# Kernel tuning notes

Hardware: AMD Instinct MI355X
Metric: run time of the kernel (lower is better)

## Reference

```python
import jax, jax.numpy as jnp
import numpy as np

B, D, H, W = 16, 512, 64, 64
K = 64  # clusters
EPS = 1e-12  # torch F.normalize eps


def _l2norm(v, axis):
    n = jnp.linalg.norm(v, axis=axis, keepdims=True)
    return v / jnp.maximum(n, EPS)


def setup_inputs() -> dict:
    key = jax.random.key(0)
    k1, k2, k3, k4 = jax.random.split(key, 4)
    x = jax.random.normal(k1, (B, D, H, W), dtype=jnp.float32)
    # conv weight/bias are independent trainable params after init; sample them
    centers = jax.random.uniform(k2, (K, D), dtype=jnp.float32)
    conv_w = 2.0 * 100.0 * centers + 0.01 * jax.random.normal(k3, (K, D), dtype=jnp.float32)
    conv_b = -100.0 * jnp.linalg.norm(centers, axis=1) + 0.01 * jax.random.normal(k4, (K,), dtype=jnp.float32)
    return {"x": x, "conv_w": conv_w, "conv_b": conv_b, "centers": centers}


def reference(x, conv_w, conv_b, centers):
    b = x.shape[0]
    x_flat = x.reshape(b, D, -1)                       # (B, D, N)
    # 1x1 conv == per-location linear over channels
    logits = jnp.einsum('bdn,kd->bkn', x_flat, conv_w) + conv_b[None, :, None]
    w = jax.nn.softmax(logits, axis=1)                 # softmax over clusters
    # vlad[b,k,d] = sum_n w[b,k,n]*(x[b,d,n] - c[k,d])
    #            = (w @ x^T)[b,k,d] - (sum_n w[b,k,n]) * c[k,d]
    wx = jnp.einsum('bkn,bdn->bkd', w, x_flat)         # (B, K, D)
    wsum = jnp.sum(w, axis=-1)                          # (B, K)
    vlad = wx - wsum[:, :, None] * centers[None]        # (B, K, D)
    vlad = _l2norm(vlad, axis=2)                        # intra-normalize
    vlad = vlad.reshape(b, -1)
    vlad = _l2norm(vlad, axis=1)                        # global L2
    return vlad
```

## Files before the change

### kernel.cpp

```cpp
#include <hip/hip_runtime.h>
#include <hip/hip_bf16.h>
#include <math.h>

#define B_ 16
#define D_ 512
#define N_ 4096
#define K_ 64

typedef __attribute__((ext_vector_type(8))) short bfrag;
typedef __attribute__((ext_vector_type(4))) float f32x4;

static __device__ __forceinline__ float bf2f(unsigned short u) {
    return __uint_as_float(((unsigned)u) << 16);
}
static __device__ __forceinline__ unsigned short f2bf(float v) {
    __hip_bfloat16 h = __float2bfloat16(v);
    union { __hip_bfloat16 h; unsigned short u; } cv; cv.h = h; return cv.u;
}
static __device__ __forceinline__ void split3(float v, unsigned short& h,
                                              unsigned short& m, unsigned short& l) {
    h = f2bf(v); float r1 = v - bf2f(h);
    m = f2bf(r1); float r2 = r1 - bf2f(m);
    l = f2bf(r2);
}
static __device__ __forceinline__ void split2(float v, unsigned short& h,
                                              unsigned short& l) {
    h = f2bf(v); l = f2bf(v - bf2f(h));
}
#define MFMA(a, b, c) __builtin_amdgcn_mfma_f32_16x16x32_bf16((a), (b), (c), 0, 0, 0)

__global__ __launch_bounds__(256) void k_prep(
    const float* __restrict__ conv_w, unsigned short* __restrict__ cwL)
{
    const int i = blockIdx.x * 256 + threadIdx.x;
    const float4 v = *(const float4*)&conv_w[i * 4];
    const float vv[4] = {v.x, v.y, v.z, v.w};
    unsigned short h[4], m[4], l[4];
    #pragma unroll
    for (int j = 0; j < 4; ++j) split3(vv[j], h[j], m[j], l[j]);
    *(ushort4*)&cwL[0 * (K_ * D_) + i * 4] = make_ushort4(h[0], h[1], h[2], h[3]);
    *(ushort4*)&cwL[1 * (K_ * D_) + i * 4] = make_ushort4(m[0], m[1], m[2], m[3]);
    *(ushort4*)&cwL[2 * (K_ * D_) + i * 4] = make_ushort4(l[0], l[1], l[2], l[3]);
}

__global__ __launch_bounds__(256) void k_logits_softmax(
    const float* __restrict__ x, const unsigned short* __restrict__ cwL,
    const float* __restrict__ conv_b,
    unsigned short* __restrict__ wh, unsigned short* __restrict__ wl,
    float* __restrict__ wsumbuf)
{
    const int b   = blockIdx.x >> 5;
    const int n0  = (blockIdx.x & 31) * 128;
    const int tid  = threadIdx.x;
    const int w    = tid >> 6;
    const int lane = tid & 63;
    const int q = lane >> 4;
    const int c = lane & 15;
    const int ktb = (w & 1) * 32;
    const int ntb = (w >> 1) * 64;

    __shared__ unsigned short cws[3][64][40];
    __shared__ unsigned short xs[3][128][40];
    __shared__ float redm[2][128];
    __shared__ float reds[2][128];

    f32x4 acc[2][4];
    #pragma unroll
    for (int kt = 0; kt < 2; ++kt)
        #pragma unroll
        for (int nt = 0; nt < 4; ++nt) acc[kt][nt] = (f32x4){0.f, 0.f, 0.f, 0.f};

    const float* xb = x + (size_t)b * D_ * N_ + n0;

    const int ks = tid >> 2;
    const int d8 = (tid & 3) * 8;

    for (int d0 = 0; d0 < D_; d0 += 32) {
        #pragma unroll
        for (int lv = 0; lv < 3; ++lv)
            *(uint4*)&cws[lv][ks][d8] =
                *(const uint4*)&cwL[lv * (K_ * D_) + ks * D_ + d0 + d8];
        #pragma unroll
        for (int i = 0; i < 4; ++i) {
            const int s  = i * 256 + tid;
            const int xn = s & 127;
            const int j  = s >> 7;
            const int Cs = ((j >> 1) ^ ((xn >> 3) & 3));
            const int dsw = (Cs * 2 + (j & 1)) * 4;
            const int dg4 = j * 4;
            unsigned short h[4], m[4], l[4];
            #pragma unroll
            for (int r = 0; r < 4; ++r) {
                const float v = xb[(size_t)(d0 + dg4 + r) * N_ + xn];
                split3(v, h[r], m[r], l[r]);
            }
            *(ushort4*)&xs[0][xn][dsw] = make_ushort4(h[0], h[1], h[2], h[3]);
            *(ushort4*)&xs[1][xn][dsw] = make_ushort4(m[0], m[1], m[2], m[3]);
            *(ushort4*)&xs[2][xn][dsw] = make_ushort4(l[0], l[1], l[2], l[3]);
        }
        __syncthreads();

        bfrag af[2][3];
        #pragma unroll
        for (int kt = 0; kt < 2; ++kt)
            #pragma unroll
            for (int lv = 0; lv < 3; ++lv)
                af[kt][lv] = *(const bfrag*)&cws[lv][ktb + kt * 16 + c][q * 8];
        #pragma unroll
        for (int nt = 0; nt < 4; ++nt) {
            const int row = ntb + nt * 16 + c;
            const int qs  = (q ^ ((row >> 3) & 3)) * 8;
            bfrag bf[3];
            #pragma unroll
            for (int lv = 0; lv < 3; ++lv)
                bf[lv] = *(const bfrag*)&xs[lv][row][qs];
            #pragma unroll
            for (int kt = 0; kt < 2; ++kt) {
                f32x4 a = acc[kt][nt];
                a = MFMA(af[kt][0], bf[0], a);
                a = MFMA(af[kt][0], bf[1], a);
                a = MFMA(af[kt][1], bf[0], a);
                a = MFMA(af[kt][1], bf[1], a);
                a = MFMA(af[kt][0], bf[2], a);
                a = MFMA(af[kt][2], bf[0], a);
                acc[kt][nt] = a;
            }
        }
        __syncthreads();
    }

    #pragma unroll
    for (int kt = 0; kt < 2; ++kt)
        #pragma unroll
        for (int r = 0; r < 4; ++r) {
            const float bias = conv_b[ktb + kt * 16 + q * 4 + r];
            #pragma unroll
            for (int nt = 0; nt < 4; ++nt) acc[kt][nt][r] += bias;
        }

    float mloc[4];
    #pragma unroll
    for (int nt = 0; nt < 4; ++nt) {
        float m = acc[0][nt][0];
        #pragma unroll
        for (int kt = 0; kt < 2; ++kt)
            #pragma unroll
            for (int r = 0; r < 4; ++r) m = fmaxf(m, acc[kt][nt][r]);
        m = fmaxf(m, __shfl_xor(m, 16));
        m = fmaxf(m, __shfl_xor(m, 32));
        mloc[nt] = m;
    }
    if (q == 0)
        #pragma unroll
        for (int nt = 0; nt < 4; ++nt) redm[w & 1][ntb + nt * 16 + c] = mloc[nt];
    __syncthreads();
    float mall[4];
    #pragma unroll
    for (int nt = 0; nt < 4; ++nt)
        mall[nt] = fmaxf(redm[0][ntb + nt * 16 + c], redm[1][ntb + nt * 16 + c]);

    float sloc[4] = {0.f, 0.f, 0.f, 0.f};
    #pragma unroll
    for (int nt = 0; nt < 4; ++nt) {
        #pragma unroll
        for (int kt = 0; kt < 2; ++kt)
            #pragma unroll
            for (int r = 0; r < 4; ++r) {
                const float e = __expf(acc[kt][nt][r] - mall[nt]);
                acc[kt][nt][r] = e;
                sloc[nt] += e;
            }
        sloc[nt] += __shfl_xor(sloc[nt], 16);
        sloc[nt] += __shfl_xor(sloc[nt], 32);
    }
    if (q == 0)
        #pragma unroll
        for (int nt = 0; nt < 4; ++nt) reds[w & 1][ntb + nt * 16 + c] = sloc[nt];
    __syncthreads();

    float wacc[2][4] = {{0.f, 0.f, 0.f, 0.f}, {0.f, 0.f, 0.f, 0.f}};
    #pragma unroll
    for (int nt = 0; nt < 4; ++nt) {
        const float inv = 1.0f / (reds[0][ntb + nt * 16 + c] + reds[1][ntb + nt * 16 + c]);
        #pragma unroll
        for (int kt = 0; kt < 2; ++kt)
            #pragma unroll
            for (int r = 0; r < 4; ++r) {
                const float v = acc[kt][nt][r] * inv;
                unsigned short hi, lo;
                split2(v, hi, lo);
                const size_t idx = ((size_t)b * K_ + ktb + kt * 16 + q * 4 + r) * N_
                                 + n0 + ntb + nt * 16 + c;
                wh[idx] = hi;
                wl[idx] = lo;
                wacc[kt][r] += v;
            }
    }
    #pragma unroll
    for (int msk = 1; msk < 16; msk <<= 1)
        #pragma unroll
        for (int kt = 0; kt < 2; ++kt)
            #pragma unroll
            for (int r = 0; r < 4; ++r)
                wacc[kt][r] += __shfl_xor(wacc[kt][r], msk);
    if (c == 0)
        #pragma unroll
        for (int kt = 0; kt < 2; ++kt)
            #pragma unroll
            for (int r = 0; r < 4; ++r)
                atomicAdd(&wsumbuf[b * K_ + ktb + kt * 16 + q * 4 + r], wacc[kt][r]);
}

__global__ __launch_bounds__(256) void k_wx(
    const float* __restrict__ x, const unsigned short* __restrict__ wh,
    const unsigned short* __restrict__ wl, float* __restrict__ vlad)
{
    const int nc = blockIdx.x & 7;
    const int dc = (blockIdx.x >> 3) & 3;
    const int b  = blockIdx.x >> 5;
    const int tid  = threadIdx.x;
    const int w    = tid >> 6;
    const int lane = tid & 63;
    const int q = lane >> 4;
    const int c = lane & 15;
    const int ktb = (w & 1) * 32;
    const int dtb = (w >> 1) * 64;

    __shared__ unsigned short ws2[2][64][40];
    __shared__ unsigned short xs2[2][128][40];

    f32x4 acc[2][4];
    #pragma unroll
    for (int kt = 0; kt < 2; ++kt)
        #pragma unroll
        for (int dt = 0; dt < 4; ++dt) acc[kt][dt] = (f32x4){0.f, 0.f, 0.f, 0.f};

    const float* xb = x + (size_t)b * D_ * N_ + (size_t)dc * 128 * N_;
    const unsigned short* whb = wh + (size_t)b * K_ * N_;
    const unsigned short* wlb = wl + (size_t)b * K_ * N_;

    const int wk = tid >> 2;
    const int wn = (tid & 3) * 8;
    const int xd = tid >> 3;
    const int xn = (tid & 7) * 4;

    const int nbase = nc * 512;
    for (int n0 = nbase; n0 < nbase + 512; n0 += 32) {
        *(uint4*)&ws2[0][wk][wn] = *(const uint4*)&whb[(size_t)wk * N_ + n0 + wn];
        *(uint4*)&ws2[1][wk][wn] = *(const uint4*)&wlb[(size_t)wk * N_ + n0 + wn];
        #pragma unroll
        for (int i = 0; i < 4; ++i) {
            const float4 v = *(const float4*)&xb[(size_t)(i * 32 + xd) * N_ + n0 + xn];
            const float vv[4] = {v.x, v.y, v.z, v.w};
            unsigned short h[4], l[4];
            #pragma unroll
            for (int j = 0; j < 4; ++j) split2(vv[j], h[j], l[j]);
            *(ushort4*)&xs2[0][i * 32 + xd][xn] = make_ushort4(h[0], h[1], h[2], h[3]);
            *(ushort4*)&xs2[1][i * 32 + xd][xn] = make_ushort4(l[0], l[1], l[2], l[3]);
        }
        __syncthreads();

        bfrag afh[2], afl[2];
        #pragma unroll
        for (int kt = 0; kt < 2; ++kt) {
            afh[kt] = *(const bfrag*)&ws2[0][ktb + kt * 16 + c][q * 8];
            afl[kt] = *(const bfrag*)&ws2[1][ktb + kt * 16 + c][q * 8];
        }
        #pragma unroll
        for (int dt = 0; dt < 4; ++dt) {
            const bfrag bh = *(const bfrag*)&xs2[0][dtb + dt * 16 + c][q * 8];
            const bfrag bl = *(const bfrag*)&xs2[1][dtb + dt * 16 + c][q * 8];
            #pragma unroll
            for (int kt = 0; kt < 2; ++kt) {
                f32x4 a = acc[kt][dt];
                a = MFMA(afh[kt], bh, a);
                a = MFMA(afh[kt], bl, a);
                a = MFMA(afl[kt], bh, a);
                acc[kt][dt] = a;
            }
        }
        __syncthreads();
    }

    #pragma unroll
    for (int kt = 0; kt < 2; ++kt)
        #pragma unroll
        for (int dt = 0; dt < 4; ++dt)
            #pragma unroll
            for (int r = 0; r < 4; ++r) {
                const int k = ktb + kt * 16 + q * 4 + r;
                const int d = dc * 128 + dtb + dt * 16 + c;
                atomicAdd(&vlad[((size_t)b * K_ + k) * D_ + d], acc[kt][dt][r]);
            }
}

__global__ __launch_bounds__(256) void k_norm(
    const float* __restrict__ wsumbuf, const float* __restrict__ vlad,
    const float* __restrict__ centers, float* __restrict__ out)
{
    const int b = blockIdx.x >> 6;
    const int k = blockIdx.x & 63;
    const int tid = threadIdx.x;

    const float wsum = wsumbuf[b * K_ + k];

    const float* vr = vlad + ((size_t)b * K_ + k) * D_;
    const float* cr = centers + k * D_;
    const float v0 = vr[tid]       - wsum * cr[tid];
    const float v1 = vr[tid + 256] - wsum * cr[tid + 256];

    float ss = v0 * v0 + v1 * v1;
    __shared__ float red2[4];
    #pragma unroll
    for (int off = 32; off > 0; off >>= 1) ss += __shfl_down(ss, off, 64);
    if ((tid & 63) == 0) red2[tid >> 6] = ss;
    __syncthreads();
    const float nrm = sqrtf(red2[0] + red2[1] + red2[2] + red2[3]);
    const float scale = 1.0f / (8.0f * fmaxf(nrm, 1e-12f));

    float* outr = out + ((size_t)b * K_ + k) * D_;
    outr[tid]       = v0 * scale;
    outr[tid + 256] = v1 * scale;
}

extern "C" void kernel_launch(void* const* d_in, const int* in_sizes, int n_in,
                              void* d_out, int out_size, void* d_ws, size_t ws_size,
                              hipStream_t stream) {
    const float* x       = (const float*)d_in[0];
    const float* conv_w  = (const float*)d_in[1];
    const float* conv_b  = (const float*)d_in[2];
    const float* centers = (const float*)d_in[3];
    float* out = (float*)d_out;

    char* wsb = (char*)d_ws;
    float* vlad            = (float*)wsb;
    float* wsumbuf         = (float*)(wsb + (2u << 20));
    unsigned short* wh     = (unsigned short*)(wsb + (3u << 20));
    unsigned short* wl     = (unsigned short*)(wsb + (11u << 20));
    unsigned short* cwL    = (unsigned short*)(wsb + (19u << 20));

    hipMemsetAsync(vlad, 0, (2u << 20) + 4096, stream);

    k_prep<<<32, 256, 0, stream>>>(conv_w, cwL);
    k_logits_softmax<<<B_ * 32, 256, 0, stream>>>(x, cwL, conv_b, wh, wl, wsumbuf);
    k_wx<<<B_ * 4 * 8, 256, 0, stream>>>(x, wh, wl, vlad);
    k_norm<<<B_ * K_, 256, 0, stream>>>(wsumbuf, vlad, centers, out);
}
```

Baseline: 237.3 us.

## Fuse logits/softmax and weighted aggregation into one kernel using LDS-resident x tiles

Merges the logits+softmax kernel and the w·xᵀ kernel into a single kernel. Each block keeps a 512×64 fp32 x tile in LDS while computing logits, then reuses that tile for the aggregation MFMAs. This removes the second global read of x and the global round-trip of the bf16 hi/lo soft-assignment weights. Per-block partial VLAD sums are written to a workspace and reduced in the normalization kernel, replacing the atomics and the large memset. The cost is about 156KB of dynamic LDS per block, which allows only one 512-thread block per CU, and two barriers per 32-channel step, so the kernel may become latency bound.

```diff
diff --git a/kernel.cpp b/kernel.cpp
--- a/kernel.cpp
+++ b/kernel.cpp
@@ -28,6 +28,17 @@
     h = f2bf(v); l = f2bf(v - bf2f(h));
 }
 #define MFMA(a, b, c) __builtin_amdgcn_mfma_f32_16x16x32_bf16((a), (b), (c), 0, 0, 0)
+
+static __device__ __forceinline__ int xf_idx(int row, int col) {
+    const int CH  = col >> 2;
+    const int CHs = ((CH - 2 * (row & 7)) & 7) | (CH & 8);
+    return row * 68 + CHs * 4 + (col & 3);
+}
+static __device__ __forceinline__ int ws_idx(int k, int n) {
+    const int CH  = n >> 3;
+    const int CHs = (CH - 2 * (k & 7)) & 7;
+    return k * 72 + CHs * 8 + (n & 7);
+}
 
 __global__ __launch_bounds__(256) void k_prep(
     const float* __restrict__ conv_w, unsigned short* __restrict__ cwL)
@@ -43,271 +54,227 @@
     *(ushort4*)&cwL[2 * (K_ * D_) + i * 4] = make_ushort4(l[0], l[1], l[2], l[3]);
 }
 
-__global__ __launch_bounds__(256) void k_logits_softmax(
+__global__ __launch_bounds__(512, 2) void k_fused(
     const float* __restrict__ x, const unsigned short* __restrict__ cwL,
-    const float* __restrict__ conv_b,
-    unsigned short* __restrict__ wh, unsigned short* __restrict__ wl,
+    const float* __restrict__ conv_b, float* __restrict__ vlad_part,
     float* __restrict__ wsumbuf)
 {
-    const int b   = blockIdx.x >> 5;
-    const int n0  = (blockIdx.x & 31) * 128;
+    const int b    = blockIdx.x >> 4;
+    const int g    = blockIdx.x & 15;
     const int tid  = threadIdx.x;
     const int w    = tid >> 6;
     const int lane = tid & 63;
-    const int q = lane >> 4;
-    const int c = lane & 15;
-    const int ktb = (w & 1) * 32;
-    const int ntb = (w >> 1) * 64;
-
-    __shared__ unsigned short cws[3][64][40];
-    __shared__ unsigned short xs[3][128][40];
-    __shared__ float redm[2][128];
-    __shared__ float reds[2][128];
-
-    f32x4 acc[2][4];
-    #pragma unroll
-    for (int kt = 0; kt < 2; ++kt)
-        #pragma unroll
-        for (int nt = 0; nt < 4; ++nt) acc[kt][nt] = (f32x4){0.f, 0.f, 0.f, 0.f};
-
-    const float* xb = x + (size_t)b * D_ * N_ + n0;
-
-    const int ks = tid >> 2;
-    const int d8 = (tid & 3) * 8;
-
-    for (int d0 = 0; d0 < D_; d0 += 32) {
-        #pragma unroll
-        for (int lv = 0; lv < 3; ++lv)
-            *(uint4*)&cws[lv][ks][d8] =
-                *(const uint4*)&cwL[lv * (K_ * D_) + ks * D_ + d0 + d8];
-        #pragma unroll
-        for (int i = 0; i < 4; ++i) {
-            const int s  = i * 256 + tid;
-            const int xn = s & 127;
-            const int j  = s >> 7;
-            const int Cs = ((j >> 1) ^ ((xn >> 3) & 3));
-            const int dsw = (Cs * 2 + (j & 1)) * 4;
-            const int dg4 = j * 4;
+    const int q    = lane >> 4;
+    const int c    = lane & 15;
+    const int kw   = w >> 1;
+    const int nw   = w & 1;
+    const int dsub = w * 4;
+
+    extern __shared__ char smem[];
+    float*          xf   = (float*)smem;
+    unsigned short* xsb  = (unsigned short*)(smem + 139264);
+    unsigned short* wsb_ = (unsigned short*)(smem + 139264);
+    float*          redm = (float*)(smem + 157696);
+    float*          reds = (float*)(smem + 158720);
+
+    f32x4 acc2[16];
+    #pragma unroll
+    for (int i = 0; i < 16; ++i) acc2[i] = (f32x4){0.f, 0.f, 0.f, 0.f};
+    float wacc[4] = {0.f, 0.f, 0.f, 0.f};
+    float bias[4];
+    #pragma unroll
+    for (int r = 0; r < 4; ++r) bias[r] = conv_b[kw * 16 + q * 4 + r];
+
+    const unsigned short* cwp = cwL + (kw * 16 + c) * D_ + q * 8;
+
+    #pragma unroll 1
+    for (int t = 0; t < 4; ++t) {
+        const int gn0 = g * 256 + t * 64;
+        const float* xb = x + (size_t)b * ((size_t)D_ * N_) + gn0 + lane;
+
+        f32x4 accA[2];
+        accA[0] = (f32x4){0.f, 0.f, 0.f, 0.f};
+        accA[1] = (f32x4){0.f, 0.f, 0.f, 0.f};
+
+        float gx[4];
+        #pragma unroll
+        for (int r = 0; r < 4; ++r) gx[r] = xb[(size_t)(dsub + r) * N_];
+
+        #pragma unroll 1
+        for (int d0 = 0; d0 < D_; d0 += 32) {
+            const bfrag af0 = *(const bfrag*)(cwp + d0);
+            const bfrag af1 = *(const bfrag*)(cwp + K_ * D_ + d0);
+            const bfrag af2 = *(const bfrag*)(cwp + 2 * K_ * D_ + d0);
+            const int dn = (d0 + 32) & (D_ - 1);
+            float nx[4];
+            #pragma unroll
+            for (int r = 0; r < 4; ++r) nx[r] = xb[(size_t)(dn + dsub + r) * N_];
+
+            #pragma unroll
+            for (int r = 0; r < 4; ++r) xf[xf_idx(d0 + dsub + r, lane)] = gx[r];
             unsigned short h[4], m[4], l[4];
             #pragma unroll
+            for (int r = 0; r < 4; ++r) split3(gx[r], h[r], m[r], l[r]);
+            {
+                const int Cs  = (dsub >> 3) ^ ((lane >> 3) & 3);
+                const int dsw = Cs * 8 + (dsub & 7);
+                *(ushort4*)&xsb[0 * 2560 + lane * 40 + dsw] = make_ushort4(h[0], h[1], h[2], h[3]);
+                *(ushort4*)&xsb[1 * 2560 + lane * 40 + dsw] = make_ushort4(m[0], m[1], m[2], m[3]);
+                *(ushort4*)&xsb[2 * 2560 + lane * 40 + dsw] = make_ushort4(l[0], l[1], l[2], l[3]);
+            }
+            __syncthreads();
+            #pragma unroll
+            for (int nt = 0; nt < 2; ++nt) {
+                const int row = nw * 32 + nt * 16 + c;
+                const int qs  = (q ^ ((row >> 3) & 3)) * 8;
+                const bfrag bf0 = *(const bfrag*)&xsb[0 * 2560 + row * 40 + qs];
+                const bfrag bf1 = *(const bfrag*)&xsb[1 * 2560 + row * 40 + qs];
+                const bfrag bf2 = *(const bfrag*)&xsb[2 * 2560 + row * 40 + qs];
+                f32x4 a = accA[nt];
+                a = MFMA(af0, bf0, a);
+                a = MFMA(af0, bf1, a);
+                a = MFMA(af1, bf0, a);
+                a = MFMA(af1, bf1, a);
+                a = MFMA(af0, bf2, a);
+                a = MFMA(af2, bf0, a);
+                accA[nt] = a;
+            }
+            __syncthreads();
+            #pragma unroll
+            for (int r = 0; r < 4; ++r) gx[r] = nx[r];
+        }
+
+        #pragma unroll
+        for (int nt = 0; nt < 2; ++nt)
+            #pragma unroll
+            for (int r = 0; r < 4; ++r) accA[nt][r] += bias[r];
+
+        {
+            float ml[2];
+            #pragma unroll
+            for (int nt = 0; nt < 2; ++nt) {
+                float mm = fmaxf(fmaxf(accA[nt][0], accA[nt][1]),
+                                 fmaxf(accA[nt][2], accA[nt][3]));
+                mm = fmaxf(mm, __shfl_xor(mm, 16));
+                mm = fmaxf(mm, __shfl_xor(mm, 32));
+                ml[nt] = mm;
+            }
+            if (q == 0) {
+                redm[kw * 64 + nw * 32 + c]      = ml[0];
+                redm[kw * 64 + nw * 32 + 16 + c] = ml[1];
+            }
+        }
+        __syncthreads();
+        float mall[2];
+        #pragma unroll
+        for (int nt = 0; nt < 2; ++nt) {
+            const int n = nw * 32 + nt * 16 + c;
+            mall[nt] = fmaxf(fmaxf(redm[n], redm[64 + n]),
+                             fmaxf(redm[128 + n], redm[192 + n]));
+        }
+        float sl[2] = {0.f, 0.f};
+        #pragma unroll
+        for (int nt = 0; nt < 2; ++nt) {
+            #pragma unroll
             for (int r = 0; r < 4; ++r) {
-                const float v = xb[(size_t)(d0 + dg4 + r) * N_ + xn];
-                split3(v, h[r], m[r], l[r]);
-            }
-            *(ushort4*)&xs[0][xn][dsw] = make_ushort4(h[0], h[1], h[2], h[3]);
-            *(ushort4*)&xs[1][xn][dsw] = make_ushort4(m[0], m[1], m[2], m[3]);
-            *(ushort4*)&xs[2][xn][dsw] = make_ushort4(l[0], l[1], l[2], l[3]);
+                const float e = __expf(accA[nt][r] - mall[nt]);
+                accA[nt][r] = e;
+                sl[nt] += e;
+            }
+            sl[nt] += __shfl_xor(sl[nt], 16);
+            sl[nt] += __shfl_xor(sl[nt], 32);
+        }
+        if (q == 0) {
+            reds[kw * 64 + nw * 32 + c]      = sl[0];
+            reds[kw * 64 + nw * 32 + 16 + c] = sl[1];
         }
         __syncthreads();
-
-        bfrag af[2][3];
-        #pragma unroll
-        for (int kt = 0; kt < 2; ++kt)
-            #pragma unroll
-            for (int lv = 0; lv < 3; ++lv)
-                af[kt][lv] = *(const bfrag*)&cws[lv][ktb + kt * 16 + c][q * 8];
-        #pragma unroll
-        for (int nt = 0; nt < 4; ++nt) {
-            const int row = ntb + nt * 16 + c;
-            const int qs  = (q ^ ((row >> 3) & 3)) * 8;
-            bfrag bf[3];
-            #pragma unroll
-            for (int lv = 0; lv < 3; ++lv)
-                bf[lv] = *(const bfrag*)&xs[lv][row][qs];
-            #pragma unroll
-            for (int kt = 0; kt < 2; ++kt) {
-                f32x4 a = acc[kt][nt];
-                a = MFMA(af[kt][0], bf[0], a);
-                a = MFMA(af[kt][0], bf[1], a);
-                a = MFMA(af[kt][1], bf[0], a);
-                a = MFMA(af[kt][1], bf[1], a);
-                a = MFMA(af[kt][0], bf[2], a);
-                a = MFMA(af[kt][2], bf[0], a);
-                acc[kt][nt] = a;
-            }
+        #pragma unroll
+        for (int nt = 0; nt < 2; ++nt) {
+            const int n = nw * 32 + nt * 16 + c;
+            const float inv = 1.0f / (reds[n] + reds[64 + n] + reds[128 + n] + reds[192 + n]);
+            #pragma unroll
+            for (int r = 0; r < 4; ++r) {
+                const float v = accA[nt][r] * inv;
+                unsigned short hi, lo;
+                split2(v, hi, lo);
+                const int k = kw * 16 + q * 4 + r;
+                wsb_[ws_idx(k, n)]        = hi;
+                wsb_[4608 + ws_idx(k, n)] = lo;
+                wacc[r] += v;
+            }
+        }
+        __syncthreads();
+
+        bfrag awh[2], awl[2];
+        #pragma unroll
+        for (int ns = 0; ns < 2; ++ns) {
+            awh[ns] = *(const bfrag*)&wsb_[ws_idx(kw * 16 + c, ns * 32 + q * 8)];
+            awl[ns] = *(const bfrag*)&wsb_[4608 + ws_idx(kw * 16 + c, ns * 32 + q * 8)];
+        }
+        #pragma unroll
+        for (int i = 0; i < 16; ++i) {
+            const int row = i * 32 + nw * 16 + c;
+            f32x4 a = acc2[i];
+            #pragma unroll
+            for (int ns = 0; ns < 2; ++ns) {
+                const float4 v0 = *(const float4*)&xf[xf_idx(row, ns * 32 + q * 8)];
+                const float4 v1 = *(const float4*)&xf[xf_idx(row, ns * 32 + q * 8 + 4)];
+                const float vv[8] = {v0.x, v0.y, v0.z, v0.w, v1.x, v1.y, v1.z, v1.w};
+                bfrag bh, bl;
+                #pragma unroll
+                for (int j = 0; j < 8; ++j) {
+                    unsigned short hh, ll;
+                    split2(vv[j], hh, ll);
+                    bh[j] = (short)hh;
+                    bl[j] = (short)ll;
+                }
+                a = MFMA(awh[ns], bh, a);
+                a = MFMA(awh[ns], bl, a);
+                a = MFMA(awl[ns], bh, a);
+            }
+            acc2[i] = a;
         }
         __syncthreads();
     }
 
     #pragma unroll
-    for (int kt = 0; kt < 2; ++kt)
-        #pragma unroll
-        for (int r = 0; r < 4; ++r) {
-            const float bias = conv_b[ktb + kt * 16 + q * 4 + r];
-            #pragma unroll
-            for (int nt = 0; nt < 4; ++nt) acc[kt][nt][r] += bias;
-        }
-
-    float mloc[4];
-    #pragma unroll
-    for (int nt = 0; nt < 4; ++nt) {
-        float m = acc[0][nt][0];
-        #pragma unroll
-        for (int kt = 0; kt < 2; ++kt)
-            #pragma unroll
-            for (int r = 0; r < 4; ++r) m = fmaxf(m, acc[kt][nt][r]);
-        m = fmaxf(m, __shfl_xor(m, 16));
-        m = fmaxf(m, __shfl_xor(m, 32));
-        mloc[nt] = m;
-    }
-    if (q == 0)
-        #pragma unroll
-        for (int nt = 0; nt < 4; ++nt) redm[w & 1][ntb + nt * 16 + c] = mloc[nt];
-    __syncthreads();
-    float mall[4];
-    #pragma unroll
-    for (int nt = 0; nt < 4; ++nt)
-        mall[nt] = fmaxf(redm[0][ntb + nt * 16 + c], redm[1][ntb + nt * 16 + c]);
-
-    float sloc[4] = {0.f, 0.f, 0.f, 0.f};
-    #pragma unroll
-    for (int nt = 0; nt < 4; ++nt) {
-        #pragma unroll
-        for (int kt = 0; kt < 2; ++kt)
-            #pragma unroll
-            for (int r = 0; r < 4; ++r) {
-                const float e = __expf(acc[kt][nt][r] - mall[nt]);
-                acc[kt][nt][r] = e;
-                sloc[nt] += e;
-            }
-        sloc[nt] += __shfl_xor(sloc[nt], 16);
-        sloc[nt] += __shfl_xor(sloc[nt], 32);
-    }
-    if (q == 0)
-        #pragma unroll
-        for (int nt = 0; nt < 4; ++nt) reds[w & 1][ntb + nt * 16 + c] = sloc[nt];
-    __syncthreads();
-
-    float wacc[2][4] = {{0.f, 0.f, 0.f, 0.f}, {0.f, 0.f, 0.f, 0.f}};
-    #pragma unroll
-    for (int nt = 0; nt < 4; ++nt) {
-        const float inv = 1.0f / (reds[0][ntb + nt * 16 + c] + reds[1][ntb + nt * 16 + c]);
-        #pragma unroll
-        for (int kt = 0; kt < 2; ++kt)
-            #pragma unroll
-            for (int r = 0; r < 4; ++r) {
-                const float v = acc[kt][nt][r] * inv;
-                unsigned short hi, lo;
-                split2(v, hi, lo);
-                const size_t idx = ((size_t)b * K_ + ktb + kt * 16 + q * 4 + r) * N_
-                                 + n0 + ntb + nt * 16 + c;
-                wh[idx] = hi;
-                wl[idx] = lo;
-                wacc[kt][r] += v;
-            }
-    }
-    #pragma unroll
     for (int msk = 1; msk < 16; msk <<= 1)
         #pragma unroll
-        for (int kt = 0; kt < 2; ++kt)
-            #pragma unroll
-            for (int r = 0; r < 4; ++r)
-                wacc[kt][r] += __shfl_xor(wacc[kt][r], msk);
+        for (int r = 0; r < 4; ++r) wacc[r] += __shfl_xor(wacc[r], msk);
     if (c == 0)
         #pragma unroll
-        for (int kt = 0; kt < 2; ++kt)
-            #pragma unroll
-            for (int r = 0; r < 4; ++r)
-                atomicAdd(&wsumbuf[b * K_ + ktb + kt * 16 + q * 4 + r], wacc[kt][r]);
-}
-
-__global__ __launch_bounds__(256) void k_wx(
-    const float* __restrict__ x, const unsigned short* __restrict__ wh,
-    const unsigned short* __restrict__ wl, float* __restrict__ vlad)
-{
-    const int nc = blockIdx.x & 7;
-    const int dc = (blockIdx.x >> 3) & 3;
-    const int b  = blockIdx.x >> 5;
-    const int tid  = threadIdx.x;
-    const int w    = tid >> 6;
-    const int lane = tid & 63;
-    const int q = lane >> 4;
-    const int c = lane & 15;
-    const int ktb = (w & 1) * 32;
-    const int dtb = (w >> 1) * 64;
-
-    __shared__ unsigned short ws2[2][64][40];
-    __shared__ unsigned short xs2[2][128][40];
-
-    f32x4 acc[2][4];
-    #pragma unroll
-    for (int kt = 0; kt < 2; ++kt)
-        #pragma unroll
-        for (int dt = 0; dt < 4; ++dt) acc[kt][dt] = (f32x4){0.f, 0.f, 0.f, 0.f};
-
-    const float* xb = x + (size_t)b * D_ * N_ + (size_t)dc * 128 * N_;
-    const unsigned short* whb = wh + (size_t)b * K_ * N_;
-    const unsigned short* wlb = wl + (size_t)b * K_ * N_;
-
-    const int wk = tid >> 2;
-    const int wn = (tid & 3) * 8;
-    const int xd = tid >> 3;
-    const int xn = (tid & 7) * 4;
-
-    const int nbase = nc * 512;
-    for (int n0 = nbase; n0 < nbase + 512; n0 += 32) {
-        *(uint4*)&ws2[0][wk][wn] = *(const uint4*)&whb[(size_t)wk * N_ + n0 + wn];
-        *(uint4*)&ws2[1][wk][wn] = *(const uint4*)&wlb[(size_t)wk * N_ + n0 + wn];
-        #pragma unroll
-        for (int i = 0; i < 4; ++i) {
-            const float4 v = *(const float4*)&xb[(size_t)(i * 32 + xd) * N_ + n0 + xn];
-            const float vv[4] = {v.x, v.y, v.z, v.w};
-            unsigned short h[4], l[4];
-            #pragma unroll
-            for (int j = 0; j < 4; ++j) split2(vv[j], h[j], l[j]);
-            *(ushort4*)&xs2[0][i * 32 + xd][xn] = make_ushort4(h[0], h[1], h[2], h[3]);
-            *(ushort4*)&xs2[1][i * 32 + xd][xn] = make_ushort4(l[0], l[1], l[2], l[3]);
-        }
-        __syncthreads();
-
-        bfrag afh[2], afl[2];
-        #pragma unroll
-        for (int kt = 0; kt < 2; ++kt) {
-            afh[kt] = *(const bfrag*)&ws2[0][ktb + kt * 16 + c][q * 8];
-            afl[kt] = *(const bfrag*)&ws2[1][ktb + kt * 16 + c][q * 8];
-        }
-        #pragma unroll
-        for (int dt = 0; dt < 4; ++dt) {
-            const bfrag bh = *(const bfrag*)&xs2[0][dtb + dt * 16 + c][q * 8];
-            const bfrag bl = *(const bfrag*)&xs2[1][dtb + dt * 16 + c][q * 8];
-            #pragma unroll
-            for (int kt = 0; kt < 2; ++kt) {
-                f32x4 a = acc[kt][dt];
-                a = MFMA(afh[kt], bh, a);
-                a = MFMA(afh[kt], bl, a);
-                a = MFMA(afl[kt], bh, a);
-                acc[kt][dt] = a;
-            }
-        }
-        __syncthreads();
-    }
-
-    #pragma unroll
-    for (int kt = 0; kt < 2; ++kt)
-        #pragma unroll
-        for (int dt = 0; dt < 4; ++dt)
-            #pragma unroll
-            for (int r = 0; r < 4; ++r) {
-                const int k = ktb + kt * 16 + q * 4 + r;
-                const int d = dc * 128 + dtb + dt * 16 + c;
-                atomicAdd(&vlad[((size_t)b * K_ + k) * D_ + d], acc[kt][dt][r]);
-            }
+        for (int r = 0; r < 4; ++r)
+            atomicAdd(&wsumbuf[b * K_ + kw * 16 + q * 4 + r], wacc[r]);
+
+    float* vp = vlad_part + ((size_t)(b * 16 + g) * K_) * D_;
+    #pragma unroll
+    for (int i = 0; i < 16; ++i)
+        #pragma unroll
+        for (int r = 0; r < 4; ++r)
+            vp[(size_t)(kw * 16 + q * 4 + r) * D_ + i * 32 + nw * 16 + c] = acc2[i][r];
 }
 
 __global__ __launch_bounds__(256) void k_norm(
-    const float* __restrict__ wsumbuf, const float* __restrict__ vlad,
+    const float* __restrict__ wsumbuf, const float* __restrict__ vlad_part,
     const float* __restrict__ centers, float* __restrict__ out)
 {
-    const int b = blockIdx.x >> 6;
-    const int k = blockIdx.x & 63;
+    const int b   = blockIdx.x >> 6;
+    const int k   = blockIdx.x & 63;
     const int tid = threadIdx.x;
 
     const float wsum = wsumbuf[b * K_ + k];
 
-    const float* vr = vlad + ((size_t)b * K_ + k) * D_;
+    const float* vp = vlad_part + ((size_t)(b * 16) * K_ + k) * D_;
+    float a0 = 0.f, a1 = 0.f;
+    #pragma unroll 4
+    for (int gg = 0; gg < 16; ++gg) {
+        a0 += vp[(size_t)gg * K_ * D_ + tid];
+        a1 += vp[(size_t)gg * K_ * D_ + tid + 256];
+    }
     const float* cr = centers + k * D_;
-    const float v0 = vr[tid]       - wsum * cr[tid];
-    const float v1 = vr[tid + 256] - wsum * cr[tid + 256];
+    const float v0 = a0 - wsum * cr[tid];
+    const float v1 = a1 - wsum * cr[tid + 256];
 
     float ss = v0 * v0 + v1 * v1;
     __shared__ float red2[4];
@@ -332,17 +299,21 @@
     const float* centers = (const float*)d_in[3];
     float* out = (float*)d_out;
 
-    char* wsb = (char*)d_ws;
-    float* vlad            = (float*)wsb;
-    float* wsumbuf         = (float*)(wsb + (2u << 20));
-    unsigned short* wh     = (unsigned short*)(wsb + (3u << 20));
-    unsigned short* wl     = (unsigned short*)(wsb + (11u << 20));
-    unsigned short* cwL    = (unsigned short*)(wsb + (19u << 20));
-
-    hipMemsetAsync(vlad, 0, (2u << 20) + 4096, stream);
+    char* wsp = (char*)d_ws;
+    float* vlad_part    = (float*)wsp;
+    float* wsumbuf      = (float*)(wsp + (32u << 20));
+    unsigned short* cwL = (unsigned short*)(wsp + (32u << 20) + (1u << 16));
+
+    hipMemsetAsync(wsumbuf, 0, B_ * K_ * sizeof(float), stream);
+
+    static bool attr_set = false;
+    if (!attr_set) {
+        (void)hipFuncSetAttribute((const void*)k_fused,
+                                  hipFuncAttributeMaxDynamicSharedMemorySize, 159744);
+        attr_set = true;
+    }
 
     k_prep<<<32, 256, 0, stream>>>(conv_w, cwL);
-    k_logits_softmax<<<B_ * 32, 256, 0, stream>>>(x, cwL, conv_b, wh, wl, wsumbuf);
-    k_wx<<<B_ * 4 * 8, 256, 0, stream>>>(x, wh, wl, vlad);
-    k_norm<<<B_ * K_, 256, 0, stream>>>(wsumbuf, vlad, centers, out);
-}
+    k_fused<<<B_ * 16, 512, 159744, stream>>>(x, cwL, conv_b, vlad_part, wsumbuf);
+    k_norm<<<B_ * K_, 256, 0, stream>>>(wsumbuf, vlad_part, centers, out);
+}
```

Measured after the change: 257.1 us. 1.08x slower.

## Interleave softmax weight hi/lo words and load conv weights directly into registers

Applied to the files above, without the earlier changes.

The softmax weights' bf16 hi and lo parts are now packed into one 32-bit word per element, so each kernel makes one coalesced store and one load instead of two separate arrays. k_wx unpacks them into the two shared-memory tiles. The logits kernel drops its shared-memory staging of the conv-weight fragments and loads them straight from global memory into registers, which frees LDS. Both kernels also gain a min-blocks-per-CU hint of 5, which may limit registers per thread and risk spills.

```diff
diff --git a/kernel.cpp b/kernel.cpp
--- a/kernel.cpp
+++ b/kernel.cpp
@@ -43,11 +43,10 @@
     *(ushort4*)&cwL[2 * (K_ * D_) + i * 4] = make_ushort4(l[0], l[1], l[2], l[3]);
 }
 
-__global__ __launch_bounds__(256) void k_logits_softmax(
+__global__ __launch_bounds__(256, 5) void k_logits_softmax(
     const float* __restrict__ x, const unsigned short* __restrict__ cwL,
     const float* __restrict__ conv_b,
-    unsigned short* __restrict__ wh, unsigned short* __restrict__ wl,
-    float* __restrict__ wsumbuf)
+    unsigned int* __restrict__ whl, float* __restrict__ wsumbuf)
 {
     const int b   = blockIdx.x >> 5;
     const int n0  = (blockIdx.x & 31) * 128;
@@ -59,7 +58,6 @@
     const int ktb = (w & 1) * 32;
     const int ntb = (w >> 1) * 64;
 
-    __shared__ unsigned short cws[3][64][40];
     __shared__ unsigned short xs[3][128][40];
     __shared__ float redm[2][128];
     __shared__ float reds[2][128];
@@ -71,15 +69,15 @@
         for (int nt = 0; nt < 4; ++nt) acc[kt][nt] = (f32x4){0.f, 0.f, 0.f, 0.f};
 
     const float* xb = x + (size_t)b * D_ * N_ + n0;
-
-    const int ks = tid >> 2;
-    const int d8 = (tid & 3) * 8;
+    const unsigned short* cwp = cwL + (ktb + c) * D_ + q * 8;
 
     for (int d0 = 0; d0 < D_; d0 += 32) {
-        #pragma unroll
-        for (int lv = 0; lv < 3; ++lv)
-            *(uint4*)&cws[lv][ks][d8] =
-                *(const uint4*)&cwL[lv * (K_ * D_) + ks * D_ + d0 + d8];
+        bfrag af[2][3];
+        #pragma unroll
+        for (int kt = 0; kt < 2; ++kt)
+            #pragma unroll
+            for (int lv = 0; lv < 3; ++lv)
+                af[kt][lv] = *(const bfrag*)(cwp + lv * (K_ * D_) + kt * 16 * D_ + d0);
         #pragma unroll
         for (int i = 0; i < 4; ++i) {
             const int s  = i * 256 + tid;
@@ -100,12 +98,6 @@
         }
         __syncthreads();
 
-        bfrag af[2][3];
-        #pragma unroll
-        for (int kt = 0; kt < 2; ++kt)
-            #pragma unroll
-            for (int lv = 0; lv < 3; ++lv)
-                af[kt][lv] = *(const bfrag*)&cws[lv][ktb + kt * 16 + c][q * 8];
         #pragma unroll
         for (int nt = 0; nt < 4; ++nt) {
             const int row = ntb + nt * 16 + c;
@@ -191,8 +183,7 @@
                 split2(v, hi, lo);
                 const size_t idx = ((size_t)b * K_ + ktb + kt * 16 + q * 4 + r) * N_
                                  + n0 + ntb + nt * 16 + c;
-                wh[idx] = hi;
-                wl[idx] = lo;
+                whl[idx] = (unsigned)hi | ((unsigned)lo << 16);
                 wacc[kt][r] += v;
             }
     }
@@ -211,9 +202,9 @@
                 atomicAdd(&wsumbuf[b * K_ + ktb + kt * 16 + q * 4 + r], wacc[kt][r]);
 }
 
-__global__ __launch_bounds__(256) void k_wx(
-    const float* __restrict__ x, const unsigned short* __restrict__ wh,
-    const unsigned short* __restrict__ wl, float* __restrict__ vlad)
+__global__ __launch_bounds__(256, 5) void k_wx(
+    const float* __restrict__ x, const unsigned int* __restrict__ whl,
+    float* __restrict__ vlad)
 {
     const int nc = blockIdx.x & 7;
     const int dc = (blockIdx.x >> 3) & 3;
@@ -236,8 +227,7 @@
         for (int dt = 0; dt < 4; ++dt) acc[kt][dt] = (f32x4){0.f, 0.f, 0.f, 0.f};
 
     const float* xb = x + (size_t)b * D_ * N_ + (size_t)dc * 128 * N_;
-    const unsigned short* whb = wh + (size_t)b * K_ * N_;
-    const unsigned short* wlb = wl + (size_t)b * K_ * N_;
+    const unsigned int* wb = whl + (size_t)b * K_ * N_;
 
     const int wk = tid >> 2;
     const int wn = (tid & 3) * 8;
@@ -246,8 +236,21 @@
 
     const int nbase = nc * 512;
     for (int n0 = nbase; n0 < nbase + 512; n0 += 32) {
-        *(uint4*)&ws2[0][wk][wn] = *(const uint4*)&whb[(size_t)wk * N_ + n0 + wn];
-        *(uint4*)&ws2[1][wk][wn] = *(const uint4*)&wlb[(size_t)wk * N_ + n0 + wn];
+        {
+            const uint4 a = *(const uint4*)&wb[(size_t)wk * N_ + n0 + wn];
+            const uint4 bq = *(const uint4*)&wb[(size_t)wk * N_ + n0 + wn + 4];
+            bfrag h8, l8;
+            h8[0] = (short)(unsigned short)a.x;  l8[0] = (short)(unsigned short)(a.x >> 16);
+            h8[1] = (short)(unsigned short)a.y;  l8[1] = (short)(unsigned short)(a.y >> 16);
+            h8[2] = (short)(unsigned short)a.z;  l8[2] = (short)(unsigned short)(a.z >> 16);
+            h8[3] = (short)(unsigned short)a.w;  l8[3] = (short)(unsigned short)(a.w >> 16);
+            h8[4] = (short)(unsigned short)bq.x; l8[4] = (short)(unsigned short)(bq.x >> 16);
+            h8[5] = (short)(unsigned short)bq.y; l8[5] = (short)(unsigned short)(bq.y >> 16);
+            h8[6] = (short)(unsigned short)bq.z; l8[6] = (short)(unsigned short)(bq.z >> 16);
+            h8[7] = (short)(unsigned short)bq.w; l8[7] = (short)(unsigned short)(bq.w >> 16);
+            *(bfrag*)&ws2[0][wk][wn] = h8;
+            *(bfrag*)&ws2[1][wk][wn] = l8;
+        }
         #pragma unroll
         for (int i = 0; i < 4; ++i) {
             const float4 v = *(const float4*)&xb[(size_t)(i * 32 + xd) * N_ + n0 + xn];
@@ -333,16 +336,15 @@
     float* out = (float*)d_out;
 
     char* wsb = (char*)d_ws;
-    float* vlad            = (float*)wsb;
-    float* wsumbuf         = (float*)(wsb + (2u << 20));
-    unsigned short* wh     = (unsigned short*)(wsb + (3u << 20));
-    unsigned short* wl     = (unsigned short*)(wsb + (11u << 20));
-    unsigned short* cwL    = (unsigned short*)(wsb + (19u << 20));
+    float* vlad         = (float*)wsb;
+    float* wsumbuf      = (float*)(wsb + (2u << 20));
+    unsigned int* whl   = (unsigned int*)(wsb + (3u << 20));
+    unsigned short* cwL = (unsigned short*)(wsb + (20u << 20));
 
     hipMemsetAsync(vlad, 0, (2u << 20) + 4096, stream);
 
     k_prep<<<32, 256, 0, stream>>>(conv_w, cwL);
-    k_logits_softmax<<<B_ * 32, 256, 0, stream>>>(x, cwL, conv_b, wh, wl, wsumbuf);
-    k_wx<<<B_ * 4 * 8, 256, 0, stream>>>(x, wh, wl, vlad);
+    k_logits_softmax<<<B_ * 32, 256, 0, stream>>>(x, cwL, conv_b, whl, wsumbuf);
+    k_wx<<<B_ * 4 * 8, 256, 0, stream>>>(x, whl, vlad);
     k_norm<<<B_ * K_, 256, 0, stream>>>(wsumbuf, vlad, centers, out);
 }
```

Result: slower. 256.9 us (+8.2%).
